# Kernel tuning notes

Measured on AMD Instinct MI355X. Metric: run time of the kernel, lower is better.

The kernel has to match this reference:

```python
import jax, jax.numpy as jnp
import numpy as np

B, H, S, D = 2, 16, 2048, 64

def setup_inputs() -> dict:
    key = jax.random.key(0)
    kq, kk, kv = jax.random.split(key, 3)
    q = jax.random.normal(kq, (B, H, S, D), dtype=jnp.float32)
    k = jax.random.normal(kk, (B, H, S, D), dtype=jnp.float32)
    v = jax.random.normal(kv, (B, H, S, D), dtype=jnp.float32)
    mask = jnp.tril(jnp.ones((S, S), dtype=bool))  # causal, broadcast over B,H
    return {"q": q, "k": k, "v": v, "mask": mask}

def reference(q, k, v, mask):
    d_k = q.shape[-1]
    # [..., num_q, num_kv]
    qk = jnp.einsum('bhqd,bhkd->bhqk', q, k) / jnp.sqrt(jnp.asarray(d_k, q.dtype))
    qk = jnp.where(mask, qk, -jnp.inf)
    attn = jax.nn.softmax(qk, axis=-1)
    return jnp.einsum('bhqk,bhkd->bhqd', attn, v)
```

## Files before the change

kernel.cpp:

```cpp
#include <hip/hip_runtime.h>

#define SS 2048
#define DD 64
#define BH 32
#define QSCALE 0.1803368801f
#define BUFS 8448

typedef __attribute__((ext_vector_type(8))) short short8;
typedef __attribute__((ext_vector_type(4))) float floatx4;

__device__ __forceinline__ short f2bf(float x) {
  union { float f; unsigned u; } un; un.f = x;
  unsigned r = (un.u + 0x7FFFu + ((un.u >> 16) & 1u)) >> 16;
  return (short)r;
}
__device__ __forceinline__ short f2bf_fast(float x) {
  union { float f; unsigned u; } un; un.f = x;
  return (short)((un.u + 0x8000u) >> 16);
}
__device__ __forceinline__ float fexp2(float x) {
  return __builtin_amdgcn_exp2f(x);
}
__device__ __forceinline__ void gload16(const short* g, short* l) {
  __builtin_amdgcn_global_load_lds(
      (const __attribute__((address_space(1))) void*)g,
      (__attribute__((address_space(3))) void*)l, 16, 0, 0);
}
#define MFMA __builtin_amdgcn_mfma_f32_16x16x32_bf16

__device__ __forceinline__ int kperm(int c) {
  return (((c >> 2) & 1) << 4) + ((c >> 3) << 2) + (c & 3);
}

__global__ __launch_bounds__(256) void prep_kv(const float* __restrict__ K,
                                               const float* __restrict__ V,
                                               short* __restrict__ Kbf,
                                               short* __restrict__ Vtp) {
  __shared__ short Ts[64][72];
  const int bh = blockIdx.x;
  const int r0 = blockIdx.y * 64;
  const int t  = threadIdx.x;
  {
    const int r = t >> 2, c = (t & 3) * 16;
    const float* g = V + ((size_t)bh * SS + r0 + r) * DD + c;
    floatx4 a = *(const floatx4*)g;
    floatx4 b = *(const floatx4*)(g + 4);
    floatx4 cc = *(const floatx4*)(g + 8);
    floatx4 dd = *(const floatx4*)(g + 12);
    short8 x0, x1;
    x0[0]=f2bf(a[0]); x0[1]=f2bf(a[1]); x0[2]=f2bf(a[2]); x0[3]=f2bf(a[3]);
    x0[4]=f2bf(b[0]); x0[5]=f2bf(b[1]); x0[6]=f2bf(b[2]); x0[7]=f2bf(b[3]);
    x1[0]=f2bf(cc[0]);x1[1]=f2bf(cc[1]);x1[2]=f2bf(cc[2]);x1[3]=f2bf(cc[3]);
    x1[4]=f2bf(dd[0]);x1[5]=f2bf(dd[1]);x1[6]=f2bf(dd[2]);x1[7]=f2bf(dd[3]);
    *(short8*)&Ts[r][c] = x0;
    *(short8*)&Ts[r][c + 8] = x1;
  }
  {
    const size_t i = ((size_t)bh * SS + r0) * DD + (size_t)t * 16;
    floatx4 a = *(const floatx4*)(K + i);
    floatx4 b = *(const floatx4*)(K + i + 4);
    floatx4 cc = *(const floatx4*)(K + i + 8);
    floatx4 dd = *(const floatx4*)(K + i + 12);
    short8 x0, x1;
    x0[0]=f2bf(a[0]); x0[1]=f2bf(a[1]); x0[2]=f2bf(a[2]); x0[3]=f2bf(a[3]);
    x0[4]=f2bf(b[0]); x0[5]=f2bf(b[1]); x0[6]=f2bf(b[2]); x0[7]=f2bf(b[3]);
    x1[0]=f2bf(cc[0]);x1[1]=f2bf(cc[1]);x1[2]=f2bf(cc[2]);x1[3]=f2bf(cc[3]);
    x1[4]=f2bf(dd[0]);x1[5]=f2bf(dd[1]);x1[6]=f2bf(dd[2]);x1[7]=f2bf(dd[3]);
    *(short8*)(Kbf + i) = x0;
    *(short8*)(Kbf + i + 8) = x1;
  }
  __syncthreads();
  {
    const int d = t >> 2, cblk = (t & 3) * 16;
    short8 y0, y1;
    #pragma unroll
    for (int jj = 0; jj < 8; ++jj) {
      const int c0 = cblk + jj, c1 = cblk + 8 + jj;
      y0[jj] = Ts[(c0 & 32) + kperm(c0 & 31)][d];
      y1[jj] = Ts[(c1 & 32) + kperm(c1 & 31)][d];
    }
    const int kt  = (r0 + cblk) >> 5;
    const int kin = cblk & 31;
    short* o = Vtp + (((size_t)bh * 64 + kt) * 64 + d) * 32 + kin;
    *(short8*)o = y0;
    *(short8*)(o + 8) = y1;
  }
}

#define TILE_COMPUTE(JJ, MODE)                                               \
  {                                                                          \
    const short* lb = bufp + (JJ) * 2176;                                    \
    const short* vb = bufp + 4352 + (JJ) * 2048;                             \
    short8 kb00 = *(const short8*)(lb + kroA);                               \
    short8 kb01 = *(const short8*)(lb + kroB);                               \
    short8 kb10 = *(const short8*)(lb + kroA + 1088);                        \
    short8 kb11 = *(const short8*)(lb + kroB + 1088);                        \
    short8 vt0 = *(const short8*)(vb + vro);                                 \
    short8 vt1 = *(const short8*)(vb + vro + 512);                           \
    short8 vt2 = *(const short8*)(vb + vro + 1024);                          \
    short8 vt3 = *(const short8*)(vb + vro + 1536);                          \
    floatx4 t0 = z, t1 = z;                                                  \
    t0 = MFMA(kb00, qa0, t0, 0, 0, 0); t0 = MFMA(kb01, qa1, t0, 0, 0, 0);    \
    t1 = MFMA(kb10, qa0, t1, 0, 0, 0); t1 = MFMA(kb11, qa1, t1, 0, 0, 0);    \
    if ((MODE) == 1) {                                                       \
      _Pragma("unroll")                                                      \
      for (int r = 0; r < 4; ++r) {                                          \
        t0[r] = (quad * 4 + r <= l16) ? t0[r] : -1e30f;                      \
        t1[r] = -1e30f;                                                      \
      }                                                                      \
    } else if ((MODE) == 2) {                                                \
      _Pragma("unroll")                                                      \
      for (int r = 0; r < 4; ++r) {                                          \
        t1[r] = (quad * 4 + r <= l16) ? t1[r] : -1e30f;                      \
      }                                                                      \
    }                                                                        \
    short8 pa;                                                               \
    _Pragma("unroll")                                                        \
    for (int r = 0; r < 4; ++r) {                                            \
      pa[r]     = f2bf_fast(fexp2(t0[r]));                                   \
      pa[4 + r] = f2bf_fast(fexp2(t1[r]));                                   \
    }                                                                        \
    sacc = MFMA(ones, pa, sacc, 0, 0, 0);                                    \
    o0 = MFMA(vt0, pa, o0, 0, 0, 0); o1 = MFMA(vt1, pa, o1, 0, 0, 0);        \
    o2 = MFMA(vt2, pa, o2, 0, 0, 0); o3 = MFMA(vt3, pa, o3, 0, 0, 0);        \
  }

__global__ __launch_bounds__(256, 4) void sdpa_fused(
    const float* __restrict__ Q, const short* __restrict__ Kbf,
    const short* __restrict__ Vtp, float* __restrict__ Og) {
  __shared__ __align__(16) short Sh[2][BUFS];

  const int tid  = threadIdx.x;
  const int w    = tid >> 6;
  const int lane = tid & 63;
  const int quad = lane >> 4;
  const int l16  = lane & 15;

  const int bh = blockIdx.x;
  const int y  = blockIdx.y;
  const int qt = (y < 16) ? (31 - y) : (y - 16);

  const size_t base = (size_t)bh * SS * DD;
  const short* kbase = Kbf + base;
  const short* vtb   = Vtp + base;

  const int kso = (lane >> 3) * 64 + (((lane & 7) ^ (lane >> 3)) * 8);
  const int vso = (lane >> 2) * 32 + (((lane & 3) ^ ((lane >> 3) & 3)) * 8);
  const int kroA = (l16 >> 3) * 544 + (l16 & 7) * 64 + ((quad ^ (l16 & 7)) * 8);
  const int kroB = (l16 >> 3) * 544 + (l16 & 7) * 64 + (((quad + 4) ^ (l16 & 7)) * 8);
  const int vro  = l16 * 32 + ((quad ^ ((l16 >> 1) & 3)) * 8);

  short8 ones;
  #pragma unroll
  for (int r = 0; r < 8; ++r) ones[r] = (short)0x3F80;
  const floatx4 z = {0.f, 0.f, 0.f, 0.f};
  const int hw = w >> 1;

  const int np = qt + 1;
  const int qA = qt * 64 + w * 16;

  {
    const short* gk = kbase + w * 512 + kso;
    gload16(gk,        &Sh[0][w * 544]);
    gload16(gk + 2048, &Sh[0][2176 + w * 544]);
    const short* gv = vtb + w * 512 + vso;
    gload16(gv,        &Sh[0][4352 + w * 512]);
    gload16(gv + 2048, &Sh[0][6400 + w * 512]);
  }

  short8 qa0, qa1;
  {
    const float* ga = Q + base + (size_t)(qA + l16) * DD + quad * 8;
    floatx4 a0 = *(const floatx4*)ga,        a1 = *(const floatx4*)(ga + 4);
    floatx4 a2 = *(const floatx4*)(ga + 32), a3 = *(const floatx4*)(ga + 36);
    #pragma unroll
    for (int r = 0; r < 4; ++r) {
      qa0[r] = f2bf(a0[r] * QSCALE); qa0[4 + r] = f2bf(a1[r] * QSCALE);
      qa1[r] = f2bf(a2[r] * QSCALE); qa1[4 + r] = f2bf(a3[r] * QSCALE);
    }
  }

  floatx4 o0 = z, o1 = z, o2 = z, o3 = z;
  floatx4 sacc = z;

  int nb = 0;
  for (int p = 0; p < np; ++p) {
    __asm__ volatile("s_waitcnt vmcnt(0)" ::: "memory");
    __syncthreads();
    const short* bufp = Sh[nb];

    if (p + 1 < np) {
      {
        const size_t go = (size_t)(p + 1) * 4096;
        const short* gk = kbase + go + w * 512 + kso;
        gload16(gk,        &Sh[nb ^ 1][w * 544]);
        gload16(gk + 2048, &Sh[nb ^ 1][2176 + w * 544]);
        const short* gv = vtb + go + w * 512 + vso;
        gload16(gv,        &Sh[nb ^ 1][4352 + w * 512]);
        gload16(gv + 2048, &Sh[nb ^ 1][6400 + w * 512]);
      }
      TILE_COMPUTE(0, 0)
      TILE_COMPUTE(1, 0)
    } else {
      #pragma unroll
      for (int jj = 0; jj < 2; ++jj) {
        if (jj < hw) {
          TILE_COMPUTE(jj, 0)
        } else if (jj == hw) {
          if (w & 1) { TILE_COMPUTE(jj, 2) }
          else       { TILE_COMPUTE(jj, 1) }
        }
      }
    }
    nb ^= 1;
  }

  const float inv = 1.0f / sacc[0];
  o0 *= inv; o1 *= inv; o2 *= inv; o3 *= inv;
  float* ra = Og + base + (size_t)(qA + l16) * DD + quad * 4;
  *(floatx4*)(ra)      = o0;
  *(floatx4*)(ra + 16) = o1;
  *(floatx4*)(ra + 32) = o2;
  *(floatx4*)(ra + 48) = o3;
}

extern "C" void kernel_launch(void* const* d_in, const int* in_sizes, int n_in,
                              void* d_out, int out_size, void* d_ws, size_t ws_size,
                              hipStream_t stream) {
  (void)in_sizes; (void)n_in; (void)out_size; (void)ws_size;
  const float* q = (const float*)d_in[0];
  const float* k = (const float*)d_in[1];
  const float* v = (const float*)d_in[2];
  float* o = (float*)d_out;

  short* Kbf = (short*)d_ws;
  short* Vtp = Kbf + (size_t)BH * SS * DD;

  prep_kv<<<dim3(BH, SS / 64), 256, 0, stream>>>(k, v, Kbf, Vtp);
  sdpa_fused<<<dim3(BH, 32), 256, 0, stream>>>(q, Kbf, Vtp, o);
}
```

Measured before the change: 132.2 us.

## Split each 64-key tile across wave pairs with 32-query blocks per wave

Each wave now owns 32 query rows and processes one 32-key half of every staged tile instead of 16 rows over both halves, so each K/V fragment read from LDS feeds two query sub-blocks. Partial outputs and row sums from the two waves sharing a query block are combined through LDS at the end before normalization and store. This cuts LDS reads per MFMA and balances diagonal-tile work, at the cost of more accumulator registers, an extra reduction step with two barriers, and idle waves on the final store.

```diff
diff --git a/kernel.cpp b/kernel.cpp
--- a/kernel.cpp
+++ b/kernel.cpp
@@ -87,7 +87,7 @@
   }
 }
 
-#define TILE_COMPUTE(JJ, MODE)                                               \
+#define TILE32(JJ, DIAG_)                                                    \
   {                                                                          \
     const short* lb = bufp + (JJ) * 2176;                                    \
     const short* vb = bufp + 4352 + (JJ) * 2048;                             \
@@ -99,30 +99,33 @@
     short8 vt1 = *(const short8*)(vb + vro + 512);                           \
     short8 vt2 = *(const short8*)(vb + vro + 1024);                          \
     short8 vt3 = *(const short8*)(vb + vro + 1536);                          \
-    floatx4 t0 = z, t1 = z;                                                  \
-    t0 = MFMA(kb00, qa0, t0, 0, 0, 0); t0 = MFMA(kb01, qa1, t0, 0, 0, 0);    \
-    t1 = MFMA(kb10, qa0, t1, 0, 0, 0); t1 = MFMA(kb11, qa1, t1, 0, 0, 0);    \
-    if ((MODE) == 1) {                                                       \
+    floatx4 tA0 = z, tA1 = z, tB0 = z, tB1 = z;                              \
+    tA0 = MFMA(kb00, qaA0, tA0, 0, 0, 0); tA0 = MFMA(kb01, qaA1, tA0, 0, 0, 0);\
+    tA1 = MFMA(kb10, qaA0, tA1, 0, 0, 0); tA1 = MFMA(kb11, qaA1, tA1, 0, 0, 0);\
+    tB0 = MFMA(kb00, qaB0, tB0, 0, 0, 0); tB0 = MFMA(kb01, qaB1, tB0, 0, 0, 0);\
+    tB1 = MFMA(kb10, qaB0, tB1, 0, 0, 0); tB1 = MFMA(kb11, qaB1, tB1, 0, 0, 0);\
+    if (DIAG_) {                                                             \
       _Pragma("unroll")                                                      \
       for (int r = 0; r < 4; ++r) {                                          \
-        t0[r] = (quad * 4 + r <= l16) ? t0[r] : -1e30f;                      \
-        t1[r] = -1e30f;                                                      \
-      }                                                                      \
-    } else if ((MODE) == 2) {                                                \
-      _Pragma("unroll")                                                      \
-      for (int r = 0; r < 4; ++r) {                                          \
-        t1[r] = (quad * 4 + r <= l16) ? t1[r] : -1e30f;                      \
+        tA0[r] = (quad * 4 + r      <= l16) ? tA0[r] : -1e30f;               \
+        tA1[r] = (quad * 4 + r + 16 <= l16) ? tA1[r] : -1e30f;               \
+        tB1[r] = (quad * 4 + r      <= l16) ? tB1[r] : -1e30f;               \
       }                                                                      \
     }                                                                        \
-    short8 pa;                                                               \
+    short8 paA, paB;                                                         \
     _Pragma("unroll")                                                        \
     for (int r = 0; r < 4; ++r) {                                            \
-      pa[r]     = f2bf_fast(fexp2(t0[r]));                                   \
-      pa[4 + r] = f2bf_fast(fexp2(t1[r]));                                   \
+      paA[r]     = f2bf_fast(fexp2(tA0[r]));                                 \
+      paA[4 + r] = f2bf_fast(fexp2(tA1[r]));                                 \
+      paB[r]     = f2bf_fast(fexp2(tB0[r]));                                 \
+      paB[4 + r] = f2bf_fast(fexp2(tB1[r]));                                 \
     }                                                                        \
-    sacc = MFMA(ones, pa, sacc, 0, 0, 0);                                    \
-    o0 = MFMA(vt0, pa, o0, 0, 0, 0); o1 = MFMA(vt1, pa, o1, 0, 0, 0);        \
-    o2 = MFMA(vt2, pa, o2, 0, 0, 0); o3 = MFMA(vt3, pa, o3, 0, 0, 0);        \
+    sA = MFMA(ones, paA, sA, 0, 0, 0);                                       \
+    sB = MFMA(ones, paB, sB, 0, 0, 0);                                       \
+    oA0 = MFMA(vt0, paA, oA0, 0, 0, 0); oA1 = MFMA(vt1, paA, oA1, 0, 0, 0);  \
+    oA2 = MFMA(vt2, paA, oA2, 0, 0, 0); oA3 = MFMA(vt3, paA, oA3, 0, 0, 0);  \
+    oB0 = MFMA(vt0, paB, oB0, 0, 0, 0); oB1 = MFMA(vt1, paB, oB1, 0, 0, 0);  \
+    oB2 = MFMA(vt2, paB, oB2, 0, 0, 0); oB3 = MFMA(vt3, paB, oB3, 0, 0, 0);  \
   }
 
 __global__ __launch_bounds__(256, 4) void sdpa_fused(
@@ -135,6 +138,8 @@
   const int lane = tid & 63;
   const int quad = lane >> 4;
   const int l16  = lane & 15;
+  const int qp   = w >> 1;
+  const int kp   = w & 1;
 
   const int bh = blockIdx.x;
   const int y  = blockIdx.y;
@@ -154,10 +159,10 @@
   #pragma unroll
   for (int r = 0; r < 8; ++r) ones[r] = (short)0x3F80;
   const floatx4 z = {0.f, 0.f, 0.f, 0.f};
-  const int hw = w >> 1;
 
   const int np = qt + 1;
-  const int qA = qt * 64 + w * 16;
+  const int qA = qt * 64 + qp * 32;
+  const int qB = qA + 16;
 
   {
     const short* gk = kbase + w * 512 + kso;
@@ -168,20 +173,26 @@
     gload16(gv + 2048, &Sh[0][6400 + w * 512]);
   }
 
-  short8 qa0, qa1;
+  short8 qaA0, qaA1, qaB0, qaB1;
   {
     const float* ga = Q + base + (size_t)(qA + l16) * DD + quad * 8;
+    const float* gb = Q + base + (size_t)(qB + l16) * DD + quad * 8;
     floatx4 a0 = *(const floatx4*)ga,        a1 = *(const floatx4*)(ga + 4);
     floatx4 a2 = *(const floatx4*)(ga + 32), a3 = *(const floatx4*)(ga + 36);
+    floatx4 b0 = *(const floatx4*)gb,        b1 = *(const floatx4*)(gb + 4);
+    floatx4 b2 = *(const floatx4*)(gb + 32), b3 = *(const floatx4*)(gb + 36);
     #pragma unroll
     for (int r = 0; r < 4; ++r) {
-      qa0[r] = f2bf(a0[r] * QSCALE); qa0[4 + r] = f2bf(a1[r] * QSCALE);
-      qa1[r] = f2bf(a2[r] * QSCALE); qa1[4 + r] = f2bf(a3[r] * QSCALE);
+      qaA0[r] = f2bf(a0[r] * QSCALE); qaA0[4 + r] = f2bf(a1[r] * QSCALE);
+      qaA1[r] = f2bf(a2[r] * QSCALE); qaA1[4 + r] = f2bf(a3[r] * QSCALE);
+      qaB0[r] = f2bf(b0[r] * QSCALE); qaB0[4 + r] = f2bf(b1[r] * QSCALE);
+      qaB1[r] = f2bf(b2[r] * QSCALE); qaB1[4 + r] = f2bf(b3[r] * QSCALE);
     }
   }
 
-  floatx4 o0 = z, o1 = z, o2 = z, o3 = z;
-  floatx4 sacc = z;
+  floatx4 oA0 = z, oA1 = z, oA2 = z, oA3 = z;
+  floatx4 oB0 = z, oB1 = z, oB2 = z, oB3 = z;
+  floatx4 sA = z, sB = z;
 
   int nb = 0;
   for (int p = 0; p < np; ++p) {
@@ -199,29 +210,47 @@
         gload16(gv,        &Sh[nb ^ 1][4352 + w * 512]);
         gload16(gv + 2048, &Sh[nb ^ 1][6400 + w * 512]);
       }
-      TILE_COMPUTE(0, 0)
-      TILE_COMPUTE(1, 0)
+      TILE32(kp, 0)
     } else {
-      #pragma unroll
-      for (int jj = 0; jj < 2; ++jj) {
-        if (jj < hw) {
-          TILE_COMPUTE(jj, 0)
-        } else if (jj == hw) {
-          if (w & 1) { TILE_COMPUTE(jj, 2) }
-          else       { TILE_COMPUTE(jj, 1) }
-        }
-      }
+      if (kp == qp) { TILE32(kp, 1) }
+      else if (kp < qp) { TILE32(kp, 0) }
     }
     nb ^= 1;
   }
 
-  const float inv = 1.0f / sacc[0];
-  o0 *= inv; o1 *= inv; o2 *= inv; o3 *= inv;
-  float* ra = Og + base + (size_t)(qA + l16) * DD + quad * 4;
-  *(floatx4*)(ra)      = o0;
-  *(floatx4*)(ra + 16) = o1;
-  *(floatx4*)(ra + 32) = o2;
-  *(floatx4*)(ra + 48) = o3;
+  __syncthreads();
+  float* lf = (float*)&Sh[0][0];
+  if (kp) {
+    floatx4* dst = (floatx4*)&lf[qp * 2048];
+    dst[0 * 64 + lane] = oA0; dst[1 * 64 + lane] = oA1;
+    dst[2 * 64 + lane] = oA2; dst[3 * 64 + lane] = oA3;
+    dst[4 * 64 + lane] = oB0; dst[5 * 64 + lane] = oB1;
+    dst[6 * 64 + lane] = oB2; dst[7 * 64 + lane] = oB3;
+    lf[4096 + qp * 128 + lane]      = sA[0];
+    lf[4096 + qp * 128 + 64 + lane] = sB[0];
+  }
+  __syncthreads();
+  if (!kp) {
+    const floatx4* src = (const floatx4*)&lf[qp * 2048];
+    oA0 += src[0 * 64 + lane]; oA1 += src[1 * 64 + lane];
+    oA2 += src[2 * 64 + lane]; oA3 += src[3 * 64 + lane];
+    oB0 += src[4 * 64 + lane]; oB1 += src[5 * 64 + lane];
+    oB2 += src[6 * 64 + lane]; oB3 += src[7 * 64 + lane];
+    const float invA = 1.0f / (sA[0] + lf[4096 + qp * 128 + lane]);
+    const float invB = 1.0f / (sB[0] + lf[4096 + qp * 128 + 64 + lane]);
+    oA0 *= invA; oA1 *= invA; oA2 *= invA; oA3 *= invA;
+    oB0 *= invB; oB1 *= invB; oB2 *= invB; oB3 *= invB;
+    float* ra = Og + base + (size_t)(qA + l16) * DD + quad * 4;
+    float* rb = Og + base + (size_t)(qB + l16) * DD + quad * 4;
+    *(floatx4*)(ra)      = oA0;
+    *(floatx4*)(ra + 16) = oA1;
+    *(floatx4*)(ra + 32) = oA2;
+    *(floatx4*)(ra + 48) = oA3;
+    *(floatx4*)(rb)      = oB0;
+    *(floatx4*)(rb + 16) = oB1;
+    *(floatx4*)(rb + 32) = oB2;
+    *(floatx4*)(rb + 48) = oB3;
+  }
 }
 
 extern "C" void kernel_launch(void* const* d_in, const int* in_sizes, int n_in,
```

New measurement: 131.5 us. Within noise of the previous version (-0.5%).
